# Performance work log

Measured on AMD Instinct MI355X. Metric: run time of the kernel, lower is better.

## Reference

```python
import jax, jax.numpy as jnp
import numpy as np

B, N, DIM, HEADS = 4, 2048, 512, 8
LN_EPS = 1e-5


def setup_inputs() -> dict:
    key = jax.random.key(0)
    ks = jax.random.split(key, 16)
    w = lambda k: jax.random.normal(k, (DIM, DIM), jnp.float32) * 0.02
    bv = lambda k: jax.random.normal(k, (DIM,), jnp.float32) * 0.02
    return {
        'x': jax.random.normal(ks[0], (B, N, DIM), jnp.float32),
        'y': jax.random.normal(ks[1], (B, N, DIM), jnp.float32),
        'Wq': w(ks[2]), 'bq': bv(ks[3]),
        'Wk': w(ks[4]), 'bk': bv(ks[5]),
        'Wvr': w(ks[6]), 'bvr': bv(ks[7]),
        'Wvd': w(ks[8]), 'bvd': bv(ks[9]),
        'g_r': jnp.ones((DIM,), jnp.float32), 'b_r': jnp.zeros((DIM,), jnp.float32),
        'g_d': jnp.ones((DIM,), jnp.float32), 'b_d': jnp.zeros((DIM,), jnp.float32),
        'Wpr': w(ks[10]), 'bpr': bv(ks[11]),
        'Wpd': w(ks[12]), 'bpd': bv(ks[13]),
        'num_heads': HEADS,
    }


def _ln(t, g, b):
    mu = jnp.mean(t, axis=-1, keepdims=True)
    var = jnp.mean(jnp.square(t - mu), axis=-1, keepdims=True)
    return (t - mu) * jax.lax.rsqrt(var + LN_EPS) * g + b


def reference(x, y, Wq, bq, Wk, bk, Wvr, bvr, Wvd, bvd,
              g_r, b_r, g_d, b_d, Wpr, bpr, Wpd, bpd, num_heads):
    Bn, Nn, C = x.shape
    D = C // num_heads
    xn = _ln(x, g_r, b_r)   # norm_r(x)
    yn = _ln(y, g_d, b_d)   # norm_d(y)

    def heads(t, W, b):  # Linear then split heads -> (B, H, N, D)
        return (t @ W.T + b).reshape(Bn, Nn, num_heads, D).transpose(0, 2, 1, 3)

    q_r = heads(yn, Wq, bq)    # query from depth-normed y
    v_r = heads(xn, Wvr, bvr)
    k_d = heads(xn, Wk, bk)
    v_d = heads(xn, Wvd, bvd)

    scale = D ** -0.5
    attn = jnp.einsum('bhnd,bhmd->bhnm', q_r, k_d) * scale  # shared QK^T
    attn_r = jax.nn.softmax(attn, axis=-1)                  # row-wise
    attn_d = jax.nn.softmax(attn.transpose(0, 1, 3, 2), axis=-1)  # col-wise (transposed)

    out_r = jnp.einsum('bhnm,bhmd->bhnd', attn_r, v_r)
    out_r = out_r.transpose(0, 2, 1, 3).reshape(Bn, Nn, C) @ Wpr.T + bpr

    o_d = jnp.einsum('bhnm,bhmd->bhnd', attn_d, v_d)
    o_d = o_d.transpose(0, 2, 1, 3).reshape(Bn, Nn, C)
    # Faithful to source quirk: extra transpose(1,2)+reshape scrambles layout.
    o_d = o_d.transpose(0, 2, 1).reshape(Bn, Nn, C)
    out_d = o_d @ Wpd.T + bpd
    return out_r, out_d
```

## Files before the change

### kernel.cpp

```cpp
#include <hip/hip_runtime.h>
#include <hip/hip_bf16.h>

typedef __hip_bfloat16 bf16;
typedef __attribute__((ext_vector_type(8))) short short8;
typedef __attribute__((ext_vector_type(4))) short short4v;
typedef __attribute__((ext_vector_type(4))) float floatx4;

static constexpr int B = 4;
static constexpr int N = 2048;
static constexpr int C = 512;
static constexpr int H = 8;
static constexpr int D = 64;

#define QK_SCALE 0.18033688011112042f

__device__ int g_flags[18];

__device__ __forceinline__ float u2f(unsigned short u) {
    return __uint_as_float(((unsigned int)u) << 16);
}
__device__ __forceinline__ unsigned short f2bf(float f) {
    unsigned int u = __float_as_uint(f);
    return (unsigned short)((u + 0x7FFFu + ((u >> 16) & 1u)) >> 16);
}
__device__ __forceinline__ float ldin(const void* p, size_t i, int f) {
    if (f == 2) return 0.0f;
    return f ? ((const float*)p)[i] : u2f(((const unsigned short*)p)[i]);
}

__device__ __forceinline__ void ld8(const void* p, size_t idx, int f, float* o) {
    if (f == 1) {
        const float4* q = (const float4*)((const float*)p + idx);
        float4 a = q[0], b2 = q[1];
        o[0] = a.x; o[1] = a.y; o[2] = a.z; o[3] = a.w;
        o[4] = b2.x; o[5] = b2.y; o[6] = b2.z; o[7] = b2.w;
    } else if (f == 0) {
        short8 s8 = *(const short8*)((const unsigned short*)p + idx);
        #pragma unroll
        for (int i = 0; i < 8; ++i) o[i] = u2f((unsigned short)s8[i]);
    } else {
        #pragma unroll
        for (int i = 0; i < 8; ++i) o[i] = 0.0f;
    }
}

__device__ __forceinline__ void gl_lds16(const unsigned short* g, unsigned short* l) {
    __builtin_amdgcn_global_load_lds(
        (const __attribute__((address_space(1))) unsigned int*)g,
        (__attribute__((address_space(3))) unsigned int*)l,
        16, 0, 0);
}

struct Ptrs { const void* p[18]; };

__global__ void detect_kernel(Ptrs ptrs) {
    int t = blockIdx.x;
    int lane = threadIdx.x;
    unsigned int v = ((const unsigned int*)ptrs.p[t])[lane];
    unsigned int e = (v >> 7) & 0xFF;
    unsigned long long mp = __ballot(e >= 96 && e <= 144);
    unsigned long long mz = __ballot(v != 0u);
    if (lane == 0)
        g_flags[t] = (mz == 0ull) ? 2 : ((__popcll(mp) >= 32) ? 0 : 1);
}

__global__ __launch_bounds__(256) void convert_w(Ptrs ptrs, bf16* dst) {
    int wsel = blockIdx.y;
    int wi = wsel < 4 ? 2 + 2 * wsel : 14 + 2 * (wsel - 4);
    int f = g_flags[wi];
    const void* src = ptrs.p[wi];
    unsigned short* out = (unsigned short*)dst + (size_t)wsel * 262144;
    int base = (blockIdx.x * 256 + threadIdx.x) * 16;
    if (f == 1) {
        const float4* s = (const float4*)((const float*)src + base);
        float4 f0 = s[0], f1 = s[1], f2 = s[2], f3 = s[3];
        uint4 o0, o1;
        o0.x = f2bf(f0.x) | ((unsigned int)f2bf(f0.y) << 16);
        o0.y = f2bf(f0.z) | ((unsigned int)f2bf(f0.w) << 16);
        o0.z = f2bf(f1.x) | ((unsigned int)f2bf(f1.y) << 16);
        o0.w = f2bf(f1.z) | ((unsigned int)f2bf(f1.w) << 16);
        o1.x = f2bf(f2.x) | ((unsigned int)f2bf(f2.y) << 16);
        o1.y = f2bf(f2.z) | ((unsigned int)f2bf(f2.w) << 16);
        o1.z = f2bf(f3.x) | ((unsigned int)f2bf(f3.y) << 16);
        o1.w = f2bf(f3.z) | ((unsigned int)f2bf(f3.w) << 16);
        *(uint4*)(out + base) = o0;
        *(uint4*)(out + base + 8) = o1;
    } else if (f == 0) {
        const uint4* s = (const uint4*)((const unsigned short*)src + base);
        uint4 a = s[0], b2 = s[1];
        *(uint4*)(out + base) = a;
        *(uint4*)(out + base + 8) = b2;
    } else {
        uint4 z = {0, 0, 0, 0};
        *(uint4*)(out + base) = z;
        *(uint4*)(out + base + 8) = z;
    }
}

__global__ __launch_bounds__(256) void ln_kernel(
    const void* __restrict__ x, const void* __restrict__ y,
    const void* __restrict__ g_r, const void* __restrict__ b_r,
    const void* __restrict__ g_d, const void* __restrict__ b_d,
    bf16* __restrict__ xn, bf16* __restrict__ yn)
{
    int tid = threadIdx.x;
    int wid = tid >> 6, lane = tid & 63;
    int row = blockIdx.x * 4 + wid;
    bool isY = row >= B * N;
    int r = isY ? row - B * N : row;
    const void* src = isY ? y : x;
    int sf = isY ? g_flags[1] : g_flags[0];
    const void* g  = isY ? g_d : g_r;
    int gf = isY ? g_flags[12] : g_flags[10];
    const void* bb = isY ? b_d : b_r;
    int bflag = isY ? g_flags[13] : g_flags[11];
    bf16* dst = (isY ? yn : xn) + (size_t)r * C;

    int col = lane * 8;
    float v[8];
    ld8(src, (size_t)r * C + col, sf, v);

    float s = 0.f, sq = 0.f;
    #pragma unroll
    for (int i = 0; i < 8; ++i) { s += v[i]; sq += v[i] * v[i]; }
    #pragma unroll
    for (int off = 1; off < 64; off <<= 1) {
        s  += __shfl_xor(s, off);
        sq += __shfl_xor(sq, off);
    }
    float mu = s * (1.0f / C);
    float var = sq * (1.0f / C) - mu * mu;
    float rs = rsqrtf(var + 1e-5f);

    float gv[8], bv[8];
    ld8(g, col, gf, gv);
    ld8(bb, col, bflag, bv);

    union { unsigned short us[8]; short8 s8; } o;
    #pragma unroll
    for (int i = 0; i < 8; ++i)
        o.us[i] = f2bf((v[i] - mu) * rs * gv[i] + bv[i]);
    *(short8*)(dst + col) = o.s8;
}

__device__ __forceinline__ void gemm_core(
    const bf16* __restrict__ A, const bf16* __restrict__ W,
    const void* __restrict__ bias, int bflag, void* __restrict__ Cout,
    int omode, float oscale, int n0, int m0)
{
    __shared__ __align__(16) unsigned short As[3][128 * 32];
    __shared__ __align__(16) unsigned short Ws[3][64 * 32];

    int tid = threadIdx.x;

    int wave = tid >> 6, lane = tid & 63;
    int wm = (wave >> 1) * 64, wn = (wave & 1) * 32;
    int quad = lane >> 4, mr = lane & 15;

    floatx4 acc[4][2] = {};

    int c0 = tid, c1 = 256 + tid;
    const unsigned short* Ag0 = (const unsigned short*)A + (size_t)(m0 + (c0 >> 2)) * 512 + (c0 & 3) * 8;
    const unsigned short* Ag1 = (const unsigned short*)A + (size_t)(m0 + (c1 >> 2)) * 512 + (c1 & 3) * 8;
    const unsigned short* Wg0 = (const unsigned short*)W + (size_t)(n0 + (c0 >> 2)) * 512 + (c0 & 3) * 8;

    auto STAGE = [&](int kt, int bsel) {
        int ko = kt * 32;
        gl_lds16(Ag0 + ko, &As[bsel][c0 * 8]);
        gl_lds16(Ag1 + ko, &As[bsel][c1 * 8]);
        gl_lds16(Wg0 + ko, &Ws[bsel][c0 * 8]);
    };

    auto GBODY = [&](int bsel, int kt) {
        if (kt < 14) {
            STAGE(kt + 2, bsel == 0 ? 2 : bsel - 1);
            asm volatile("s_waitcnt vmcnt(6)" ::: "memory");
        } else if (kt == 14) {
            asm volatile("s_waitcnt vmcnt(3)" ::: "memory");
        } else {
            asm volatile("s_waitcnt vmcnt(0)" ::: "memory");
        }
        __builtin_amdgcn_s_barrier();
        __builtin_amdgcn_sched_barrier(0);

        short8 af[4], bfr[2];
        #pragma unroll
        for (int i = 0; i < 4; ++i)
            af[i] = *(const short8*)&As[bsel][(wm + i * 16 + mr) * 32 + quad * 8];
        #pragma unroll
        for (int j = 0; j < 2; ++j)
            bfr[j] = *(const short8*)&Ws[bsel][(wn + j * 16 + mr) * 32 + quad * 8];
        #pragma unroll
        for (int i = 0; i < 4; ++i)
            #pragma unroll
            for (int j = 0; j < 2; ++j)
                acc[i][j] = __builtin_amdgcn_mfma_f32_16x16x32_bf16(
                    af[i], bfr[j], acc[i][j], 0, 0, 0);

        __builtin_amdgcn_sched_barrier(0);
        __builtin_amdgcn_s_barrier();
    };

    STAGE(0, 0);
    STAGE(1, 1);
    for (int g = 0; g < 5; ++g) {
        int kt = g * 3;
        GBODY(0, kt);
        GBODY(1, kt + 1);
        GBODY(2, kt + 2);
    }
    GBODY(0, 15);

    float bv[2];
    #pragma unroll
    for (int j = 0; j < 2; ++j)
        bv[j] = ldin(bias, n0 + wn + j * 16 + mr, bflag);
    #pragma unroll
    for (int i = 0; i < 4; ++i) {
        #pragma unroll
        for (int j = 0; j < 2; ++j) {
            int o = n0 + wn + j * 16 + mr;
            #pragma unroll
            for (int reg = 0; reg < 4; ++reg) {
                int r = m0 + wm + i * 16 + quad * 4 + reg;
                float val = (acc[i][j][reg] + bv[j]) * oscale;
                if (omode == 0) {
                    ((bf16*)Cout)[(size_t)r * 512 + o] = __float2bfloat16(val);
                } else if (omode == 1) {
                    ((float*)Cout)[(size_t)r * 512 + o] = val;
                } else {
                    int batch = r >> 11, nn = r & 2047;
                    ((bf16*)Cout)[((size_t)(batch * 512 + o)) * 2048 + nn] =
                        __float2bfloat16(val);
                }
            }
        }
    }
}

__device__ __forceinline__ void swz_nm(int& n0, int& m0) {
    m0 = (blockIdx.x * 8 + (blockIdx.y >> 3)) * 128;
    n0 = (blockIdx.y & 7) * 64;
}

__global__ __launch_bounds__(256) void gemm_stage(
    const bf16* __restrict__ xn, const bf16* __restrict__ yn,
    const bf16* __restrict__ wts, Ptrs ptrs,
    bf16* __restrict__ q, bf16* __restrict__ k,
    bf16* __restrict__ vrT, bf16* __restrict__ vdT)
{
    int z = blockIdx.z;
    const bf16* A = (z == 0) ? yn : xn;
    const bf16* W = wts + (size_t)z * 262144;
    int bi = 3 + 2 * z;
    void* Cout = (z == 0) ? (void*)q : (z == 1) ? (void*)k
               : (z == 2) ? (void*)vrT : (void*)vdT;
    int omode = (z < 2) ? 0 : 2;
    float oscale = (z == 0) ? QK_SCALE : 1.0f;
    int n0, m0;
    swz_nm(n0, m0);
    gemm_core(A, W, ptrs.p[bi], g_flags[bi], Cout, omode, oscale, n0, m0);
}

__global__ __launch_bounds__(256) void gemm_out(
    const bf16* __restrict__ Or, const bf16* __restrict__ Ad,
    const bf16* __restrict__ wts, Ptrs ptrs,
    float* __restrict__ out0, float* __restrict__ out1)
{
    int z = blockIdx.z;
    const bf16* A = z ? Ad : Or;
    const bf16* W = wts + (size_t)(4 + z) * 262144;
    int bi = 15 + 2 * z;
    int n0, m0;
    swz_nm(n0, m0);
    gemm_core(A, W, ptrs.p[bi], g_flags[bi], z ? (void*)out1 : (void*)out0,
              1, 1.0f, n0, m0);
}

__global__ __launch_bounds__(256) void flash_mfma(
    const bf16* __restrict__ qm, const bf16* __restrict__ km,
    const bf16* __restrict__ vrT, const bf16* __restrict__ vdT,
    bf16* __restrict__ Or, bf16* __restrict__ Ad)
{
    __shared__ __align__(16) unsigned short Ks[2][64 * 64];
    __shared__ __align__(16) unsigned short Vs[2][64 * 64];

    int phys = blockIdx.x + 32 * blockIdx.y + 256 * blockIdx.z;
    int s = phys >> 3;
    int qblk = s & 31;
    int gidx = (phys & 7) + ((s >> 5) << 3);
    int pass = gidx >> 5;
    int b = (gidx >> 3) & 3;
    int h = gidx & 7;

    const bf16* Q  = pass ? km : qm;
    const bf16* K  = pass ? qm : km;
    const bf16* Vt = pass ? vdT : vrT;
    bf16* Out = pass ? Ad : Or;

    int tid = threadIdx.x;
    int wave = tid >> 6, lane = tid & 63;
    int quad = lane >> 4, mr = lane & 15;
    int m8 = mr & 7;
    int qw = qblk * 64 + wave * 16;

    const unsigned short* Qb = (const unsigned short*)Q + ((size_t)(b * N + qw + mr)) * C + h * D;
    short8 qf0 = *(const short8*)(Qb + quad * 8);
    short8 qf1 = *(const short8*)(Qb + 32 + quad * 8);

    floatx4 Oacc[4] = {};
    floatx4 lacc = {};

    short4v ones;
    {
        union { unsigned int u[2]; short4v s4; } cv;
        cv.u[0] = 0x3F803F80u; cv.u[1] = 0x3F803F80u;
        ones = cv.s4;
    }

    int c0 = tid, c1 = 256 + tid;
    int r0 = c0 >> 3, cs0 = c0 & 7;
    int r1 = c1 >> 3, cs1 = c1 & 7;
    const unsigned short* Kb  = (const unsigned short*)K + ((size_t)b * N) * C + h * D;
    const unsigned short* Vtb = (const unsigned short*)Vt + ((size_t)(b * 512 + h * 64)) * 2048;
    const unsigned short* sk0 = Kb + (size_t)r0 * C + ((cs0 ^ (r0 & 7)) << 3);
    const unsigned short* sk1 = Kb + (size_t)r1 * C + ((cs1 ^ (r1 & 7)) << 3);
    const unsigned short* sv0 = Vtb + (size_t)r0 * 2048 + ((cs0 ^ (r0 & 7)) << 3);
    const unsigned short* sv1 = Vtb + (size_t)r1 * 2048 + ((cs1 ^ (r1 & 7)) << 3);

    auto STAGE = [&](int bsel) {
        gl_lds16(sk0, &Ks[bsel][c0 * 8]);
        gl_lds16(sk1, &Ks[bsel][c1 * 8]);
        gl_lds16(sv0, &Vs[bsel][c0 * 8]);
        gl_lds16(sv1, &Vs[bsel][c1 * 8]);
        sk0 += 64 * C; sk1 += 64 * C; sv0 += 64; sv1 += 64;
    };

    int skc0 = (quad ^ m8) << 3;
    int skc1 = ((quad + 4) ^ m8) << 3;
    int vq = quad >> 1, vlo = (quad & 1) * 4;

    auto BODY = [&](int cur, bool last) {
        __builtin_amdgcn_s_barrier();
        if (!last) {
            STAGE(cur ^ 1);
            asm volatile("s_waitcnt vmcnt(4)" ::: "memory");
        } else {
            asm volatile("s_waitcnt vmcnt(0)" ::: "memory");
        }
        __builtin_amdgcn_sched_barrier(0);

        floatx4 tac[4] = {};
        __builtin_amdgcn_s_setprio(1);
        #pragma unroll
        for (int t = 0; t < 4; ++t) {
            const unsigned short* kr = &Ks[cur][(t * 16 + mr) * 64];
            short8 kf0 = *(const short8*)(kr + skc0);
            short8 kf1 = *(const short8*)(kr + skc1);
            tac[t] = __builtin_amdgcn_mfma_f32_16x16x32_bf16(kf0, qf0, tac[t], 0, 0, 0);
            tac[t] = __builtin_amdgcn_mfma_f32_16x16x32_bf16(kf1, qf1, tac[t], 0, 0, 0);
        }
        __builtin_amdgcn_s_setprio(0);

        short4v pa[4];
        #pragma unroll
        for (int t = 0; t < 4; ++t) {
            float p0, p1, p2, p3;
            asm("v_exp_f32 %0, %1" : "=v"(p0) : "v"(tac[t][0]));
            asm("v_exp_f32 %0, %1" : "=v"(p1) : "v"(tac[t][1]));
            asm("v_exp_f32 %0, %1" : "=v"(p2) : "v"(tac[t][2]));
            asm("v_exp_f32 %0, %1" : "=v"(p3) : "v"(tac[t][3]));
            unsigned int u0, u1;
            asm("v_cvt_pk_bf16_f32 %0, %1, %2" : "=v"(u0) : "v"(p0), "v"(p1));
            asm("v_cvt_pk_bf16_f32 %0, %1, %2" : "=v"(u1) : "v"(p2), "v"(p3));
            union { unsigned int u[2]; short4v s4; } cv;
            cv.u[0] = u0; cv.u[1] = u1;
            pa[t] = cv.s4;
        }

        __builtin_amdgcn_s_setprio(1);
        #pragma unroll
        for (int t = 0; t < 4; ++t) {
            int vslot = (((2 * t + vq) ^ m8) << 3) + vlo;
            #pragma unroll
            for (int j = 0; j < 4; ++j) {
                short4v vb = *(const short4v*)&Vs[cur][(j * 16 + mr) * 64 + vslot];
                Oacc[j] = __builtin_amdgcn_mfma_f32_16x16x16bf16_1k(
                    pa[t], vb, Oacc[j], 0, 0, 0);
            }
            lacc = __builtin_amdgcn_mfma_f32_16x16x16bf16_1k(pa[t], ones, lacc, 0, 0, 0);
        }
        __builtin_amdgcn_s_setprio(0);
        __builtin_amdgcn_sched_barrier(0);
    };

    STAGE(0);
    for (int kt2 = 0; kt2 < 15; ++kt2) {
        BODY(0, false);
        BODY(1, false);
    }
    BODY(0, false);
    BODY(1, true);

    float inv[4];
    #pragma unroll
    for (int r = 0; r < 4; ++r)
        inv[r] = 1.0f / lacc[r];

    if (pass == 0) {
        #pragma unroll
        for (int t = 0; t < 4; ++t)
            #pragma unroll
            for (int r = 0; r < 4; ++r) {
                int n = qw + quad * 4 + r;
                Out[((size_t)(b * N + n)) * C + h * D + t * 16 + mr] =
                    __float2bfloat16(Oacc[t][r] * inv[r]);
            }
    } else {
        size_t bbase = (size_t)b * N * C;
        #pragma unroll
        for (int t = 0; t < 4; ++t)
            #pragma unroll
            for (int r = 0; r < 4; ++r) {
                int n = qw + quad * 4 + r;
                int c = h * D + t * 16 + mr;
                Out[bbase + (size_t)(c * 4 + (n >> 9)) * 512 + (n & 511)] =
                    __float2bfloat16(Oacc[t][r] * inv[r]);
            }
    }
}

extern "C" void kernel_launch(void* const* d_in, const int* in_sizes, int n_in,
                              void* d_out, int out_size, void* d_ws, size_t ws_size,
                              hipStream_t stream)
{
    const void* x   = d_in[0];
    const void* y   = d_in[1];
    const void* g_r = d_in[10];
    const void* b_r = d_in[11];
    const void* g_d = d_in[12];
    const void* b_d = d_in[13];

    Ptrs ptrs;
    for (int i = 0; i < 18; ++i) ptrs.p[i] = d_in[i];

    const size_t SL = (size_t)B * N * C;

    char* wsb = (char*)d_ws;
    bf16* q   = (bf16*)wsb;
    bf16* k   = (bf16*)(wsb + 8ull * 1024 * 1024);
    bf16* vrT = (bf16*)(wsb + 16ull * 1024 * 1024);
    bf16* vdT = (bf16*)(wsb + 24ull * 1024 * 1024);
    bf16* xn  = (bf16*)(wsb + 32ull * 1024 * 1024);
    bf16* yn  = (bf16*)(wsb + 40ull * 1024 * 1024);
    bf16* wts = (bf16*)(wsb + 48ull * 1024 * 1024);
    bf16* Or = xn;
    bf16* Ad = yn;

    float* out0 = (float*)d_out;
    float* out1 = (float*)d_out + SL;

    detect_kernel<<<18, 64, 0, stream>>>(ptrs);
    convert_w<<<dim3(64, 6), 256, 0, stream>>>(ptrs, wts);
    ln_kernel<<<2 * B * N / 4, 256, 0, stream>>>(x, y, g_r, b_r, g_d, b_d, xn, yn);

    gemm_stage<<<dim3(8, 64, 4), 256, 0, stream>>>(xn, yn, wts, ptrs, q, k, vrT, vdT);

    dim3 fg(32, 8, 8);
    flash_mfma<<<fg, 256, 0, stream>>>(q, k, vrT, vdT, Or, Ad);

    gemm_out<<<dim3(8, 64, 2), 256, 0, stream>>>(Or, Ad, wts, ptrs, out0, out1);
}
```

Measured before the change: 276.1 us.

## Widen GEMM K-tile with swizzled LDS and double the flash block to 512 threads

```diff
diff --git a/kernel.cpp b/kernel.cpp
--- a/kernel.cpp
+++ b/kernel.cpp
@@ -148,68 +148,73 @@
     const void* __restrict__ bias, int bflag, void* __restrict__ Cout,
     int omode, float oscale, int n0, int m0)
 {
-    __shared__ __align__(16) unsigned short As[3][128 * 32];
-    __shared__ __align__(16) unsigned short Ws[3][64 * 32];
+    __shared__ __align__(16) unsigned short As[2][128 * 64];
+    __shared__ __align__(16) unsigned short Ws[2][64 * 64];
 
     int tid = threadIdx.x;
-
     int wave = tid >> 6, lane = tid & 63;
     int wm = (wave >> 1) * 64, wn = (wave & 1) * 32;
     int quad = lane >> 4, mr = lane & 15;
+    int m8 = mr & 7;
 
     floatx4 acc[4][2] = {};
 
-    int c0 = tid, c1 = 256 + tid;
-    const unsigned short* Ag0 = (const unsigned short*)A + (size_t)(m0 + (c0 >> 2)) * 512 + (c0 & 3) * 8;
-    const unsigned short* Ag1 = (const unsigned short*)A + (size_t)(m0 + (c1 >> 2)) * 512 + (c1 & 3) * 8;
-    const unsigned short* Wg0 = (const unsigned short*)W + (size_t)(n0 + (c0 >> 2)) * 512 + (c0 & 3) * 8;
-
-    auto STAGE = [&](int kt, int bsel) {
-        int ko = kt * 32;
-        gl_lds16(Ag0 + ko, &As[bsel][c0 * 8]);
-        gl_lds16(Ag1 + ko, &As[bsel][c1 * 8]);
-        gl_lds16(Wg0 + ko, &Ws[bsel][c0 * 8]);
+    const unsigned short* Asrc[4];
+    const unsigned short* Wsrc[2];
+    #pragma unroll
+    for (int i = 0; i < 4; ++i) {
+        int c = i * 256 + tid, row = c >> 3, sg = c & 7;
+        Asrc[i] = (const unsigned short*)A + (size_t)(m0 + row) * 512 + ((sg ^ (row & 7)) << 3);
+    }
+    #pragma unroll
+    for (int j = 0; j < 2; ++j) {
+        int c = j * 256 + tid, row = c >> 3, sg = c & 7;
+        Wsrc[j] = (const unsigned short*)W + (size_t)(n0 + row) * 512 + ((sg ^ (row & 7)) << 3);
+    }
+
+    auto STAGE = [&](int w, int bsel) {
+        int ko = w * 64;
+        #pragma unroll
+        for (int i = 0; i < 4; ++i)
+            gl_lds16(Asrc[i] + ko, &As[bsel][(i * 256 + tid) * 8]);
+        #pragma unroll
+        for (int j = 0; j < 2; ++j)
+            gl_lds16(Wsrc[j] + ko, &Ws[bsel][(j * 256 + tid) * 8]);
     };
 
-    auto GBODY = [&](int bsel, int kt) {
-        if (kt < 14) {
-            STAGE(kt + 2, bsel == 0 ? 2 : bsel - 1);
-            asm volatile("s_waitcnt vmcnt(6)" ::: "memory");
-        } else if (kt == 14) {
-            asm volatile("s_waitcnt vmcnt(3)" ::: "memory");
-        } else {
-            asm volatile("s_waitcnt vmcnt(0)" ::: "memory");
+    auto WBODY = [&](int bsel, int w) {
+        asm volatile("s_waitcnt vmcnt(0)" ::: "memory");
+        __builtin_amdgcn_s_barrier();
+        if (w < 7)
+            STAGE(w + 1, bsel ^ 1);
+        __builtin_amdgcn_sched_barrier(0);
+
+        #pragma unroll
+        for (int kk = 0; kk < 2; ++kk) {
+            int sl = ((kk * 4 + quad) ^ m8) << 3;
+            short8 af[4], bfr[2];
+            #pragma unroll
+            for (int i = 0; i < 4; ++i)
+                af[i] = *(const short8*)&As[bsel][(wm + i * 16 + mr) * 64 + sl];
+            #pragma unroll
+            for (int j = 0; j < 2; ++j)
+                bfr[j] = *(const short8*)&Ws[bsel][(wn + j * 16 + mr) * 64 + sl];
+            #pragma unroll
+            for (int i = 0; i < 4; ++i)
+                #pragma unroll
+                for (int j = 0; j < 2; ++j)
+                    acc[i][j] = __builtin_amdgcn_mfma_f32_16x16x32_bf16(
+                        af[i], bfr[j], acc[i][j], 0, 0, 0);
         }
-        __builtin_amdgcn_s_barrier();
         __builtin_amdgcn_sched_barrier(0);
-
-        short8 af[4], bfr[2];
-        #pragma unroll
-        for (int i = 0; i < 4; ++i)
-            af[i] = *(const short8*)&As[bsel][(wm + i * 16 + mr) * 32 + quad * 8];
-        #pragma unroll
-        for (int j = 0; j < 2; ++j)
-            bfr[j] = *(const short8*)&Ws[bsel][(wn + j * 16 + mr) * 32 + quad * 8];
-        #pragma unroll
-        for (int i = 0; i < 4; ++i)
-            #pragma unroll
-            for (int j = 0; j < 2; ++j)
-                acc[i][j] = __builtin_amdgcn_mfma_f32_16x16x32_bf16(
-                    af[i], bfr[j], acc[i][j], 0, 0, 0);
-
-        __builtin_amdgcn_sched_barrier(0);
-        __builtin_amdgcn_s_barrier();
     };
 
     STAGE(0, 0);
-    STAGE(1, 1);
-    for (int g = 0; g < 5; ++g) {
-        int kt = g * 3;
-        GBODY(0, kt);
-        GBODY(1, kt + 1);
-        GBODY(2, kt + 2);
-    }
-    GBODY(0, 15);
+    #pragma unroll
+    for (int g = 0; g < 4; ++g) {
+        WBODY(0, 2 * g);
+        WBODY(1, 2 * g + 1);
+    }
 
     float bv[2];
     #pragma unroll
@@ -243,7 +248,7 @@
     n0 = (blockIdx.y & 7) * 64;
 }
 
-__global__ __launch_bounds__(256) void gemm_stage(
+__global__ __launch_bounds__(256, 3) void gemm_stage(
     const bf16* __restrict__ xn, const bf16* __restrict__ yn,
     const bf16* __restrict__ wts, Ptrs ptrs,
     bf16* __restrict__ q, bf16* __restrict__ k,
@@ -262,7 +267,7 @@
     gemm_core(A, W, ptrs.p[bi], g_flags[bi], Cout, omode, oscale, n0, m0);
 }
 
-__global__ __launch_bounds__(256) void gemm_out(
+__global__ __launch_bounds__(256, 3) void gemm_out(
     const bf16* __restrict__ Or, const bf16* __restrict__ Ad,
     const bf16* __restrict__ wts, Ptrs ptrs,
     float* __restrict__ out0, float* __restrict__ out1)
@@ -277,7 +282,7 @@
               1, 1.0f, n0, m0);
 }
 
-__global__ __launch_bounds__(256) void flash_mfma(
+__global__ __launch_bounds__(512, 8) void flash_mfma(
     const bf16* __restrict__ qm, const bf16* __restrict__ km,
     const bf16* __restrict__ vrT, const bf16* __restrict__ vdT,
     bf16* __restrict__ Or, bf16* __restrict__ Ad)
@@ -285,10 +290,10 @@
     __shared__ __align__(16) unsigned short Ks[2][64 * 64];
     __shared__ __align__(16) unsigned short Vs[2][64 * 64];
 
-    int phys = blockIdx.x + 32 * blockIdx.y + 256 * blockIdx.z;
+    int phys = blockIdx.x + 16 * blockIdx.y + 128 * blockIdx.z;
     int s = phys >> 3;
-    int qblk = s & 31;
-    int gidx = (phys & 7) + ((s >> 5) << 3);
+    int qblk = s & 15;
+    int gidx = (phys & 7) + ((s >> 4) << 3);
     int pass = gidx >> 5;
     int b = (gidx >> 3) & 3;
     int h = gidx & 7;
@@ -302,7 +307,7 @@
     int wave = tid >> 6, lane = tid & 63;
     int quad = lane >> 4, mr = lane & 15;
     int m8 = mr & 7;
-    int qw = qblk * 64 + wave * 16;
+    int qw = qblk * 128 + wave * 16;
 
     const unsigned short* Qb = (const unsigned short*)Q + ((size_t)(b * N + qw + mr)) * C + h * D;
     short8 qf0 = *(const short8*)(Qb + quad * 8);
@@ -318,22 +323,16 @@
         ones = cv.s4;
     }
 
-    int c0 = tid, c1 = 256 + tid;
-    int r0 = c0 >> 3, cs0 = c0 & 7;
-    int r1 = c1 >> 3, cs1 = c1 & 7;
+    int r0 = tid >> 3, cs0 = tid & 7;
     const unsigned short* Kb  = (const unsigned short*)K + ((size_t)b * N) * C + h * D;
     const unsigned short* Vtb = (const unsigned short*)Vt + ((size_t)(b * 512 + h * 64)) * 2048;
     const unsigned short* sk0 = Kb + (size_t)r0 * C + ((cs0 ^ (r0 & 7)) << 3);
-    const unsigned short* sk1 = Kb + (size_t)r1 * C + ((cs1 ^ (r1 & 7)) << 3);
     const unsigned short* sv0 = Vtb + (size_t)r0 * 2048 + ((cs0 ^ (r0 & 7)) << 3);
-    const unsigned short* sv1 = Vtb + (size_t)r1 * 2048 + ((cs1 ^ (r1 & 7)) << 3);
 
     auto STAGE = [&](int bsel) {
-        gl_lds16(sk0, &Ks[bsel][c0 * 8]);
-        gl_lds16(sk1, &Ks[bsel][c1 * 8]);
-        gl_lds16(sv0, &Vs[bsel][c0 * 8]);
-        gl_lds16(sv1, &Vs[bsel][c1 * 8]);
-        sk0 += 64 * C; sk1 += 64 * C; sv0 += 64; sv1 += 64;
+        gl_lds16(sk0, &Ks[bsel][tid * 8]);
+        gl_lds16(sv0, &Vs[bsel][tid * 8]);
+        sk0 += 64 * C; sv0 += 64;
     };
 
     int skc0 = (quad ^ m8) << 3;
@@ -341,13 +340,10 @@
     int vq = quad >> 1, vlo = (quad & 1) * 4;
 
     auto BODY = [&](int cur, bool last) {
+        asm volatile("s_waitcnt vmcnt(0)" ::: "memory");
         __builtin_amdgcn_s_barrier();
-        if (!last) {
+        if (!last)
             STAGE(cur ^ 1);
-            asm volatile("s_waitcnt vmcnt(4)" ::: "memory");
-        } else {
-            asm volatile("s_waitcnt vmcnt(0)" ::: "memory");
-        }
         __builtin_amdgcn_sched_barrier(0);
 
         floatx4 tac[4] = {};
@@ -466,8 +462,8 @@
 
     gemm_stage<<<dim3(8, 64, 4), 256, 0, stream>>>(xn, yn, wts, ptrs, q, k, vrT, vdT);
 
-    dim3 fg(32, 8, 8);
-    flash_mfma<<<fg, 256, 0, stream>>>(q, k, vrT, vdT, Or, Ad);
+    dim3 fg(16, 8, 8);
+    flash_mfma<<<fg, 512, 0, stream>>>(q, k, vrT, vdT, Or, Ad);
 
     gemm_out<<<dim3(8, 64, 2), 256, 0, stream>>>(Or, Ad, wts, ptrs, out0, out1);
 }
```

Measured after the change: 264.8 us. 1.04x faster.
